# Optimization experiments

Measured on AMD Instinct MI355X. Metric: run time of the kernel, lower is better.

The kernel has to match this reference:

```python
import jax, jax.numpy as jnp
import numpy as np

B, C, H, W = 4, 512, 64, 64
D = C // 8  # inter_channels = 64


def setup_inputs() -> dict:
    key = jax.random.key(0)
    ks = jax.random.split(key, 10)
    s = 1.0 / np.sqrt(C)
    so = 1.0 / np.sqrt(D)
    return {
        "x": jax.random.normal(ks[0], (B, C, H, W), dtype=jnp.float32),
        "Wq": jax.random.normal(ks[1], (D, C), dtype=jnp.float32) * s,
        "bq": jnp.zeros((D,), dtype=jnp.float32),
        "Wk": jax.random.normal(ks[2], (D, C), dtype=jnp.float32) * s,
        "bk": jnp.zeros((D,), dtype=jnp.float32),
        "Wv": jax.random.normal(ks[3], (D, C), dtype=jnp.float32) * s,
        "bv": jnp.zeros((D,), dtype=jnp.float32),
        "Wo": jax.random.normal(ks[4], (C, D), dtype=jnp.float32) * so,
        "bo": jnp.zeros((C,), dtype=jnp.float32),
        "gamma": jnp.zeros((1,), dtype=jnp.float32),
    }


def reference(x, Wq, bq, Wk, bk, Wv, bv, Wo, bo, gamma):
    b, c, h, w = x.shape
    n = h * w
    xf = x.reshape(b, c, n)  # (B, C, N)
    # 1x1 convs == channel-mixing matmuls
    q = jnp.einsum("dc,bcn->bnd", Wq, xf) + bq              # (B, N, D)
    k = jnp.einsum("dc,bcn->bdn", Wk, xf) + bk[:, None]      # (B, D, N)
    v = jnp.einsum("dc,bcn->bnd", Wv, xf) + bv               # (B, N, D)
    scores = jnp.einsum("bnd,bdm->bnm", q, k)                # (B, N, N)
    weights = jax.nn.softmax(scores, axis=-1)
    attended = jnp.einsum("bnm,bmd->bnd", weights, v)        # (B, N, D)
    out = jnp.einsum("cd,bnd->bcn", Wo, attended) + bo[:, None]
    out = out.reshape(b, c, h, w)
    return gamma[0] * out + x
```

## Files before the change

### kernel.cpp

```cpp
#include <hip/hip_runtime.h>

#define NB 4
#define CH 512
#define NN 4096
#define DD 64

typedef __attribute__((ext_vector_type(8))) short bf16x8;
typedef __attribute__((ext_vector_type(4))) float f32x4;

#define MFMA(a, b, c) __builtin_amdgcn_mfma_f32_16x16x32_bf16((a), (b), (c), 0, 0, 0)

__device__ inline unsigned short f2bf(float f) {
    unsigned int u = __builtin_bit_cast(unsigned int, f);
    unsigned int r = u + 0x7fffu + ((u >> 16) & 1u);
    return (unsigned short)(r >> 16);
}

__device__ inline float bf2f(unsigned short u) {
    return __builtin_bit_cast(float, ((unsigned int)u) << 16);
}

__device__ inline bf16x8 ld8(const unsigned short* p) {
    return *reinterpret_cast<const bf16x8*>(p);
}

__global__ __launch_bounds__(256) void convert_w(
    const float* __restrict__ Wq, const float* __restrict__ Wk,
    const float* __restrict__ Wv, const float* __restrict__ Wo,
    unsigned short* __restrict__ oq, unsigned short* __restrict__ ok,
    unsigned short* __restrict__ ov, unsigned short* __restrict__ oo) {
    int i = blockIdx.x * 256 + threadIdx.x;
    oq[i] = f2bf(Wq[i]);
    ok[i] = f2bf(Wk[i]);
    ov[i] = f2bf(Wv[i]);
    oo[i] = f2bf(Wo[i]);
}

__global__ __launch_bounds__(256) void qkv_kernel(
    const float* __restrict__ x,
    const unsigned short* __restrict__ Wq, const unsigned short* __restrict__ Wk,
    const unsigned short* __restrict__ Wv,
    const float* __restrict__ bq, const float* __restrict__ bk, const float* __restrict__ bv,
    unsigned short* __restrict__ Q, unsigned short* __restrict__ K,
    unsigned short* __restrict__ VT) {
    const int b = blockIdx.x >> 8;
    const int n0 = (blockIdx.x & 255) * 16;
    const int t = threadIdx.x;
    const int lane = t & 63, w = t >> 6;
    const int l15 = lane & 15, g = lane >> 4;

    __shared__ char smraw[36864];
    unsigned short (*sxT)[520] = (unsigned short(*)[520])smraw;
    float* red = (float*)smraw;

    {
        const int cbase = t >> 2;
        const int nq = (t & 3) * 4;
#pragma unroll
        for (int p = 0; p < 8; ++p) {
            int c = p * 64 + cbase;
            float4 v = *reinterpret_cast<const float4*>(
                &x[((size_t)(b * CH + c)) * NN + n0 + nq]);
            sxT[nq + 0][c] = f2bf(v.x);
            sxT[nq + 1][c] = f2bf(v.y);
            sxT[nq + 2][c] = f2bf(v.z);
            sxT[nq + 3][c] = f2bf(v.w);
        }
    }
    __syncthreads();

    f32x4 accQ[4], accK[4], accV[4];
    const f32x4 z = {0.f, 0.f, 0.f, 0.f};
#pragma unroll
    for (int i = 0; i < 4; ++i) { accQ[i] = z; accK[i] = z; accV[i] = z; }

    const int wc = w * 128;
#pragma unroll
    for (int i = 0; i < 4; ++i) {
        int c = wc + i * 32 + 8 * g;
        bf16x8 ax = ld8(&sxT[l15][c]);
#pragma unroll
        for (int dt = 0; dt < 4; ++dt) {
            int d = dt * 16 + l15;
            accQ[dt] = MFMA(ax, ld8(&Wq[d * CH + c]), accQ[dt]);
            accK[dt] = MFMA(ax, ld8(&Wk[d * CH + c]), accK[dt]);
            accV[dt] = MFMA(ld8(&Wv[d * CH + c]), ax, accV[dt]);
        }
    }
    __syncthreads();

    if (w > 0) {
        float* dst = &red[((w - 1) * 64 + lane) * 48];
#pragma unroll
        for (int i = 0; i < 4; ++i) {
            *reinterpret_cast<f32x4*>(&dst[i * 4]) = accQ[i];
            *reinterpret_cast<f32x4*>(&dst[16 + i * 4]) = accK[i];
            *reinterpret_cast<f32x4*>(&dst[32 + i * 4]) = accV[i];
        }
    }
    __syncthreads();
    if (w == 0) {
#pragma unroll
        for (int ww = 0; ww < 3; ++ww) {
            const float* src = &red[(ww * 64 + lane) * 48];
#pragma unroll
            for (int i = 0; i < 4; ++i) {
                accQ[i] += *reinterpret_cast<const f32x4*>(&src[i * 4]);
                accK[i] += *reinterpret_cast<const f32x4*>(&src[16 + i * 4]);
                accV[i] += *reinterpret_cast<const f32x4*>(&src[32 + i * 4]);
            }
        }
#pragma unroll
        for (int dt = 0; dt < 4; ++dt) {
            int d = dt * 16 + l15;
            float biasq = bq[d], biask = bk[d];
#pragma unroll
            for (int r = 0; r < 4; ++r) {
                int n = n0 + 4 * g + r;
                Q[((size_t)b * NN + n) * DD + d] = f2bf(accQ[dt][r] + biasq);
                K[((size_t)b * NN + n) * DD + d] = f2bf(accK[dt][r] + biask);
            }
        }
#pragma unroll
        for (int dt = 0; dt < 4; ++dt) {
#pragma unroll
            for (int r = 0; r < 4; ++r) {
                int d = dt * 16 + 4 * g + r;
                VT[((size_t)b * DD + d) * NN + n0 + l15] = f2bf(accV[dt][r] + bv[d]);
            }
        }
    }
}

__global__ __launch_bounds__(256) void attn_kernel(
    const unsigned short* __restrict__ Q, const unsigned short* __restrict__ K,
    const unsigned short* __restrict__ VT,
    unsigned short* __restrict__ PO, float* __restrict__ PML, int KVLEN) {
    const int s = blockIdx.x >> 8;
    const int bq_ = blockIdx.x & 255;
    const int b = bq_ >> 6;
    const int n0 = (bq_ & 63) * 64;
    const int t = threadIdx.x;
    const int lane = t & 63, w = t >> 6;
    const int l15 = lane & 15, g = lane >> 4;

    __shared__ unsigned short sK[64][72];
    __shared__ unsigned short sVT[64][72];
    __shared__ unsigned short sP[4][16][76];

    const int qrow = n0 + 16 * w + l15;
    bf16x8 qf0 = ld8(&Q[((size_t)b * NN + qrow) * DD + 0 + 8 * g]);
    bf16x8 qf1 = ld8(&Q[((size_t)b * NN + qrow) * DD + 32 + 8 * g]);

    f32x4 oacc[4];
    const f32x4 z = {0.f, 0.f, 0.f, 0.f};
#pragma unroll
    for (int i = 0; i < 4; ++i) oacc[i] = z;
    float m_run[4], l_run[4];
#pragma unroll
    for (int r = 0; r < 4; ++r) { m_run[r] = -1e30f; l_run[r] = 0.f; }

    const int kv_begin = s * KVLEN;
    const int kv_end = kv_begin + KVLEN;
    for (int m0 = kv_begin; m0 < kv_end; m0 += 64) {
        {
            int row = t >> 2, c16 = (t & 3) * 16;
            const unsigned short* kp = &K[((size_t)b * NN + m0 + row) * DD + c16];
            *reinterpret_cast<bf16x8*>(&sK[row][c16]) = ld8(kp);
            *reinterpret_cast<bf16x8*>(&sK[row][c16 + 8]) = ld8(kp + 8);
            const unsigned short* vp = &VT[((size_t)b * DD + row) * NN + m0 + c16];
            *reinterpret_cast<bf16x8*>(&sVT[row][c16]) = ld8(vp);
            *reinterpret_cast<bf16x8*>(&sVT[row][c16 + 8]) = ld8(vp + 8);
        }
        __syncthreads();

        f32x4 sv[4];
#pragma unroll
        for (int ct = 0; ct < 4; ++ct) sv[ct] = z;
#pragma unroll
        for (int ct = 0; ct < 4; ++ct) {
            bf16x8 kf0 = ld8(&sK[ct * 16 + l15][0 + 8 * g]);
            sv[ct] = MFMA(qf0, kf0, sv[ct]);
            bf16x8 kf1 = ld8(&sK[ct * 16 + l15][32 + 8 * g]);
            sv[ct] = MFMA(qf1, kf1, sv[ct]);
        }

        float corr[4];
#pragma unroll
        for (int r = 0; r < 4; ++r) {
            float mx = fmaxf(fmaxf(sv[0][r], sv[1][r]), fmaxf(sv[2][r], sv[3][r]));
#pragma unroll
            for (int d_ = 8; d_ >= 1; d_ >>= 1) mx = fmaxf(mx, __shfl_xor(mx, d_, 64));
            float mnew = fmaxf(m_run[r], mx);
            float c_ = __expf(m_run[r] - mnew);
            float rs = 0.f;
#pragma unroll
            for (int ct = 0; ct < 4; ++ct) {
                float p = __expf(sv[ct][r] - mnew);
                sv[ct][r] = p;
                rs += p;
            }
#pragma unroll
            for (int d_ = 8; d_ >= 1; d_ >>= 1) rs += __shfl_xor(rs, d_, 64);
            l_run[r] = l_run[r] * c_ + rs;
            m_run[r] = mnew;
            corr[r] = c_;
        }
#pragma unroll
        for (int dt = 0; dt < 4; ++dt)
#pragma unroll
            for (int r = 0; r < 4; ++r) oacc[dt][r] *= corr[r];

#pragma unroll
        for (int ct = 0; ct < 4; ++ct)
#pragma unroll
            for (int r = 0; r < 4; ++r)
                sP[w][4 * g + r][ct * 16 + l15] = f2bf(sv[ct][r]);

#pragma unroll
        for (int kk = 0; kk < 2; ++kk) {
            bf16x8 pf = ld8(&sP[w][l15][kk * 32 + 8 * g]);
#pragma unroll
            for (int dt = 0; dt < 4; ++dt) {
                bf16x8 vf = ld8(&sVT[dt * 16 + l15][kk * 32 + 8 * g]);
                oacc[dt] = MFMA(pf, vf, oacc[dt]);
            }
        }
        __syncthreads();
    }

#pragma unroll
    for (int r = 0; r < 4; ++r) {
        int n = n0 + 16 * w + 4 * g + r;
        size_t rowidx = (size_t)s * NB * NN + (size_t)b * NN + n;
#pragma unroll
        for (int dt = 0; dt < 4; ++dt)
            PO[rowidx * DD + dt * 16 + l15] = f2bf(oacc[dt][r]);
        if (l15 == 0) {
            PML[rowidx * 2 + 0] = m_run[r];
            PML[rowidx * 2 + 1] = l_run[r];
        }
    }
}

__global__ __launch_bounds__(256) void out_fused(
    const unsigned short* __restrict__ Wo, const unsigned short* __restrict__ PO,
    const float* __restrict__ PML, const float* __restrict__ bo,
    const float* __restrict__ gamma, const float* __restrict__ x,
    float* __restrict__ out, int S) {
    const int bid = blockIdx.x;
    const int b = bid >> 8;
    const int rest = bid & 255;
    const int n0 = (rest >> 2) * 64;
    const int c0 = (rest & 3) * 128;
    const int t = threadIdx.x;
    const int lane = t & 63, w = t >> 6;
    const int l15 = lane & 15, g = lane >> 4;

    __shared__ unsigned short sATT[64][72];

    {
        const int row = t >> 2;
        const int dq = (t & 3) * 16;
        const size_t base = (size_t)b * NN + n0 + row;
        float m = -1e30f;
        for (int s = 0; s < S; ++s)
            m = fmaxf(m, PML[((size_t)s * NB * NN + base) * 2]);
        float acc[16];
#pragma unroll
        for (int j = 0; j < 16; ++j) acc[j] = 0.f;
        float l = 0.f;
        for (int s = 0; s < S; ++s) {
            size_t rowidx = (size_t)s * NB * NN + base;
            float ms = PML[rowidx * 2 + 0];
            float ls = PML[rowidx * 2 + 1];
            float wgt = __expf(ms - m);
            l += wgt * ls;
            bf16x8 a0 = ld8(&PO[rowidx * DD + dq]);
            bf16x8 a1 = ld8(&PO[rowidx * DD + dq + 8]);
#pragma unroll
            for (int j = 0; j < 8; ++j) {
                acc[j] += wgt * bf2f((unsigned short)a0[j]);
                acc[8 + j] += wgt * bf2f((unsigned short)a1[j]);
            }
        }
        float inv = 1.f / l;
        bf16x8 o0, o1;
#pragma unroll
        for (int j = 0; j < 8; ++j) {
            o0[j] = (short)f2bf(acc[j] * inv);
            o1[j] = (short)f2bf(acc[8 + j] * inv);
        }
        *reinterpret_cast<bf16x8*>(&sATT[row][dq]) = o0;
        *reinterpret_cast<bf16x8*>(&sATT[row][dq + 8]) = o1;
    }
    __syncthreads();

    const int cw = c0 + w * 32;
    f32x4 acc2[2][4];
    const f32x4 z = {0.f, 0.f, 0.f, 0.f};
#pragma unroll
    for (int i = 0; i < 2; ++i)
#pragma unroll
        for (int j = 0; j < 4; ++j) acc2[i][j] = z;

#pragma unroll
    for (int kk = 0; kk < 2; ++kk) {
        bf16x8 af[2], bfr[4];
#pragma unroll
        for (int ct = 0; ct < 2; ++ct)
            af[ct] = ld8(&Wo[(cw + ct * 16 + l15) * DD + kk * 32 + 8 * g]);
#pragma unroll
        for (int nt = 0; nt < 4; ++nt)
            bfr[nt] = ld8(&sATT[nt * 16 + l15][kk * 32 + 8 * g]);
#pragma unroll
        for (int ct = 0; ct < 2; ++ct)
#pragma unroll
            for (int nt = 0; nt < 4; ++nt) acc2[ct][nt] = MFMA(af[ct], bfr[nt], acc2[ct][nt]);
    }

    float gm = gamma[0];
#pragma unroll
    for (int ct = 0; ct < 2; ++ct) {
        int c = cw + ct * 16 + 4 * g;
#pragma unroll
        for (int r = 0; r < 4; ++r) {
            float bias = bo[c + r];
#pragma unroll
            for (int nt = 0; nt < 4; ++nt) {
                int n = n0 + nt * 16 + l15;
                size_t idx = ((size_t)b * CH + c + r) * NN + n;
                out[idx] = gm * (acc2[ct][nt][r] + bias) + x[idx];
            }
        }
    }
}

extern "C" void kernel_launch(void* const* d_in, const int* in_sizes, int n_in,
                              void* d_out, int out_size, void* d_ws, size_t ws_size,
                              hipStream_t stream) {
    const float* x = (const float*)d_in[0];
    const float* Wq = (const float*)d_in[1];
    const float* bq = (const float*)d_in[2];
    const float* Wk = (const float*)d_in[3];
    const float* bk = (const float*)d_in[4];
    const float* Wv = (const float*)d_in[5];
    const float* bv = (const float*)d_in[6];
    const float* Wo = (const float*)d_in[7];
    const float* bo = (const float*)d_in[8];
    const float* gamma = (const float*)d_in[9];
    float* out = (float*)d_out;

    char* ws = (char*)d_ws;
    unsigned short* Wq_bf = (unsigned short*)(ws + 0);
    unsigned short* Wk_bf = (unsigned short*)(ws + 65536);
    unsigned short* Wv_bf = (unsigned short*)(ws + 131072);
    unsigned short* Wo_bf = (unsigned short*)(ws + 196608);
    unsigned short* Qb = (unsigned short*)(ws + 262144);
    unsigned short* Kb = (unsigned short*)(ws + 262144 + 2097152);
    unsigned short* VTb = (unsigned short*)(ws + 262144 + 2 * 2097152);
    const size_t po_off = 262144 + 3ull * 2097152;

    int S = 8;
    while (S > 1 &&
           ws_size < po_off + (size_t)S * (2097152ull + 131072ull))
        S >>= 1;
    unsigned short* PO = (unsigned short*)(ws + po_off);
    float* PML = (float*)(ws + po_off + (size_t)S * 2097152ull);

    hipLaunchKernelGGL(convert_w, dim3(128), dim3(256), 0, stream,
                       Wq, Wk, Wv, Wo, Wq_bf, Wk_bf, Wv_bf, Wo_bf);
    hipLaunchKernelGGL(qkv_kernel, dim3(1024), dim3(256), 0, stream,
                       x, Wq_bf, Wk_bf, Wv_bf, bq, bk, bv, Qb, Kb, VTb);
    hipLaunchKernelGGL(attn_kernel, dim3(256 * S), dim3(256), 0, stream,
                       Qb, Kb, VTb, PO, PML, NN / S);
    hipLaunchKernelGGL(out_fused, dim3(1024), dim3(256), 0, stream,
                       Wo_bf, PO, PML, bo, gamma, x, out, S);
}
```

Baseline: 214.4 us.

## Prefetch KV tiles, lazy softmax rescale, parallel QKV reduction, fewer splits

The attention kernel now loads the next K/V tile into registers while the current tile is being computed. It rescales the running max lazily, only when some row's new max exceeds the stored one by more than 8, and it defers the row-sum shuffle reduction to the end of the kernel. P is converted to bf16 by truncation instead of round-to-nearest. In the QKV kernel the cross-wave reduction and output writes are split across all four waves instead of being done by wave 0 alone, and the KV split count drops from 8 to 4, giving fewer partial outputs to merge but fewer blocks per launch.

```diff
diff --git a/kernel.cpp b/kernel.cpp
--- a/kernel.cpp
+++ b/kernel.cpp
@@ -14,6 +14,10 @@
     unsigned int u = __builtin_bit_cast(unsigned int, f);
     unsigned int r = u + 0x7fffu + ((u >> 16) & 1u);
     return (unsigned short)(r >> 16);
+}
+
+__device__ inline unsigned short f2bf_trunc(float f) {
+    return (unsigned short)(__builtin_bit_cast(unsigned int, f) >> 16);
 }
 
 __device__ inline float bf2f(unsigned short u) {
@@ -49,9 +53,9 @@
     const int lane = t & 63, w = t >> 6;
     const int l15 = lane & 15, g = lane >> 4;
 
-    __shared__ char smraw[36864];
+    __shared__ char smraw[49152];
     unsigned short (*sxT)[520] = (unsigned short(*)[520])smraw;
-    float* red = (float*)smraw;
+    float (*red)[4][64][12] = (float(*)[4][64][12])smraw;
 
     {
         const int cbase = t >> 2;
@@ -89,45 +93,38 @@
     }
     __syncthreads();
 
-    if (w > 0) {
-        float* dst = &red[((w - 1) * 64 + lane) * 48];
-#pragma unroll
-        for (int i = 0; i < 4; ++i) {
-            *reinterpret_cast<f32x4*>(&dst[i * 4]) = accQ[i];
-            *reinterpret_cast<f32x4*>(&dst[16 + i * 4]) = accK[i];
-            *reinterpret_cast<f32x4*>(&dst[32 + i * 4]) = accV[i];
-        }
+#pragma unroll
+    for (int dt = 0; dt < 4; ++dt) {
+        float* dst = &red[dt][w][lane][0];
+        *reinterpret_cast<f32x4*>(dst + 0) = accQ[dt];
+        *reinterpret_cast<f32x4*>(dst + 4) = accK[dt];
+        *reinterpret_cast<f32x4*>(dst + 8) = accV[dt];
     }
     __syncthreads();
-    if (w == 0) {
-#pragma unroll
-        for (int ww = 0; ww < 3; ++ww) {
-            const float* src = &red[(ww * 64 + lane) * 48];
-#pragma unroll
-            for (int i = 0; i < 4; ++i) {
-                accQ[i] += *reinterpret_cast<const f32x4*>(&src[i * 4]);
-                accK[i] += *reinterpret_cast<const f32x4*>(&src[16 + i * 4]);
-                accV[i] += *reinterpret_cast<const f32x4*>(&src[32 + i * 4]);
-            }
-        }
-#pragma unroll
-        for (int dt = 0; dt < 4; ++dt) {
-            int d = dt * 16 + l15;
-            float biasq = bq[d], biask = bk[d];
-#pragma unroll
-            for (int r = 0; r < 4; ++r) {
-                int n = n0 + 4 * g + r;
-                Q[((size_t)b * NN + n) * DD + d] = f2bf(accQ[dt][r] + biasq);
-                K[((size_t)b * NN + n) * DD + d] = f2bf(accK[dt][r] + biask);
-            }
-        }
-#pragma unroll
-        for (int dt = 0; dt < 4; ++dt) {
-#pragma unroll
-            for (int r = 0; r < 4; ++r) {
-                int d = dt * 16 + 4 * g + r;
-                VT[((size_t)b * DD + d) * NN + n0 + l15] = f2bf(accV[dt][r] + bv[d]);
-            }
+
+    f32x4 q = *reinterpret_cast<const f32x4*>(&red[w][0][lane][0]);
+    f32x4 k = *reinterpret_cast<const f32x4*>(&red[w][0][lane][4]);
+    f32x4 v = *reinterpret_cast<const f32x4*>(&red[w][0][lane][8]);
+#pragma unroll
+    for (int src = 1; src < 4; ++src) {
+        const float* sp = &red[w][src][lane][0];
+        q += *reinterpret_cast<const f32x4*>(sp + 0);
+        k += *reinterpret_cast<const f32x4*>(sp + 4);
+        v += *reinterpret_cast<const f32x4*>(sp + 8);
+    }
+    {
+        int d = w * 16 + l15;
+        float biasq = bq[d], biask = bk[d];
+#pragma unroll
+        for (int r = 0; r < 4; ++r) {
+            int n = n0 + 4 * g + r;
+            Q[((size_t)b * NN + n) * DD + d] = f2bf(q[r] + biasq);
+            K[((size_t)b * NN + n) * DD + d] = f2bf(k[r] + biask);
+        }
+#pragma unroll
+        for (int r = 0; r < 4; ++r) {
+            int dv = w * 16 + 4 * g + r;
+            VT[((size_t)b * DD + dv) * NN + n0 + l15] = f2bf(v[r] + bv[dv]);
         }
     }
 }
@@ -156,23 +153,35 @@
     const f32x4 z = {0.f, 0.f, 0.f, 0.f};
 #pragma unroll
     for (int i = 0; i < 4; ++i) oacc[i] = z;
-    float m_run[4], l_run[4];
-#pragma unroll
-    for (int r = 0; r < 4; ++r) { m_run[r] = -1e30f; l_run[r] = 0.f; }
+    float m_run[4], l_part[4];
+#pragma unroll
+    for (int r = 0; r < 4; ++r) { m_run[r] = -1e30f; l_part[r] = 0.f; }
 
     const int kv_begin = s * KVLEN;
     const int kv_end = kv_begin + KVLEN;
+    const int srow = t >> 2, sc16 = (t & 3) * 16;
+
+    bf16x8 pk0, pk1, pv0, pv1;
+    {
+        const unsigned short* kp = &K[((size_t)b * NN + kv_begin + srow) * DD + sc16];
+        pk0 = ld8(kp); pk1 = ld8(kp + 8);
+        const unsigned short* vp = &VT[((size_t)b * DD + srow) * NN + kv_begin + sc16];
+        pv0 = ld8(vp); pv1 = ld8(vp + 8);
+    }
+
     for (int m0 = kv_begin; m0 < kv_end; m0 += 64) {
-        {
-            int row = t >> 2, c16 = (t & 3) * 16;
-            const unsigned short* kp = &K[((size_t)b * NN + m0 + row) * DD + c16];
-            *reinterpret_cast<bf16x8*>(&sK[row][c16]) = ld8(kp);
-            *reinterpret_cast<bf16x8*>(&sK[row][c16 + 8]) = ld8(kp + 8);
-            const unsigned short* vp = &VT[((size_t)b * DD + row) * NN + m0 + c16];
-            *reinterpret_cast<bf16x8*>(&sVT[row][c16]) = ld8(vp);
-            *reinterpret_cast<bf16x8*>(&sVT[row][c16 + 8]) = ld8(vp + 8);
-        }
+        *reinterpret_cast<bf16x8*>(&sK[srow][sc16]) = pk0;
+        *reinterpret_cast<bf16x8*>(&sK[srow][sc16 + 8]) = pk1;
+        *reinterpret_cast<bf16x8*>(&sVT[srow][sc16]) = pv0;
+        *reinterpret_cast<bf16x8*>(&sVT[srow][sc16 + 8]) = pv1;
         __syncthreads();
+
+        if (m0 + 64 < kv_end) {
+            const unsigned short* kp = &K[((size_t)b * NN + m0 + 64 + srow) * DD + sc16];
+            pk0 = ld8(kp); pk1 = ld8(kp + 8);
+            const unsigned short* vp = &VT[((size_t)b * DD + srow) * NN + m0 + 64 + sc16];
+            pv0 = ld8(vp); pv1 = ld8(vp + 8);
+        }
 
         f32x4 sv[4];
 #pragma unroll
@@ -185,37 +194,42 @@
             sv[ct] = MFMA(qf1, kf1, sv[ct]);
         }
 
-        float corr[4];
-#pragma unroll
-        for (int r = 0; r < 4; ++r) {
-            float mx = fmaxf(fmaxf(sv[0][r], sv[1][r]), fmaxf(sv[2][r], sv[3][r]));
-#pragma unroll
-            for (int d_ = 8; d_ >= 1; d_ >>= 1) mx = fmaxf(mx, __shfl_xor(mx, d_, 64));
-            float mnew = fmaxf(m_run[r], mx);
-            float c_ = __expf(m_run[r] - mnew);
-            float rs = 0.f;
-#pragma unroll
-            for (int ct = 0; ct < 4; ++ct) {
-                float p = __expf(sv[ct][r] - mnew);
-                sv[ct][r] = p;
-                rs += p;
+        float ownmax[4];
+        bool ok = true;
+#pragma unroll
+        for (int r = 0; r < 4; ++r) {
+            ownmax[r] = fmaxf(fmaxf(sv[0][r], sv[1][r]), fmaxf(sv[2][r], sv[3][r]));
+            ok = ok && (ownmax[r] <= m_run[r] + 8.f);
+        }
+        if (!__all(ok)) {
+#pragma unroll
+            for (int r = 0; r < 4; ++r) {
+                float mx = ownmax[r];
+#pragma unroll
+                for (int d_ = 8; d_ >= 1; d_ >>= 1) mx = fmaxf(mx, __shfl_xor(mx, d_, 64));
+                float mnew = fmaxf(m_run[r], mx);
+                float c_ = __expf(m_run[r] - mnew);
+                m_run[r] = mnew;
+                l_part[r] *= c_;
+#pragma unroll
+                for (int dt = 0; dt < 4; ++dt) oacc[dt][r] *= c_;
             }
-#pragma unroll
-            for (int d_ = 8; d_ >= 1; d_ >>= 1) rs += __shfl_xor(rs, d_, 64);
-            l_run[r] = l_run[r] * c_ + rs;
-            m_run[r] = mnew;
-            corr[r] = c_;
-        }
-#pragma unroll
-        for (int dt = 0; dt < 4; ++dt)
-#pragma unroll
-            for (int r = 0; r < 4; ++r) oacc[dt][r] *= corr[r];
+        }
+#pragma unroll
+        for (int r = 0; r < 4; ++r) {
+            float p0 = __expf(sv[0][r] - m_run[r]);
+            float p1 = __expf(sv[1][r] - m_run[r]);
+            float p2 = __expf(sv[2][r] - m_run[r]);
+            float p3 = __expf(sv[3][r] - m_run[r]);
+            sv[0][r] = p0; sv[1][r] = p1; sv[2][r] = p2; sv[3][r] = p3;
+            l_part[r] += (p0 + p1) + (p2 + p3);
+        }
 
 #pragma unroll
         for (int ct = 0; ct < 4; ++ct)
 #pragma unroll
             for (int r = 0; r < 4; ++r)
-                sP[w][4 * g + r][ct * 16 + l15] = f2bf(sv[ct][r]);
+                sP[w][4 * g + r][ct * 16 + l15] = f2bf_trunc(sv[ct][r]);
 
 #pragma unroll
         for (int kk = 0; kk < 2; ++kk) {
@@ -231,6 +245,9 @@
 
 #pragma unroll
     for (int r = 0; r < 4; ++r) {
+        float lt = l_part[r];
+#pragma unroll
+        for (int d_ = 8; d_ >= 1; d_ >>= 1) lt += __shfl_xor(lt, d_, 64);
         int n = n0 + 16 * w + 4 * g + r;
         size_t rowidx = (size_t)s * NB * NN + (size_t)b * NN + n;
 #pragma unroll
@@ -238,7 +255,7 @@
             PO[rowidx * DD + dt * 16 + l15] = f2bf(oacc[dt][r]);
         if (l15 == 0) {
             PML[rowidx * 2 + 0] = m_run[r];
-            PML[rowidx * 2 + 1] = l_run[r];
+            PML[rowidx * 2 + 1] = lt;
         }
     }
 }
@@ -361,7 +378,7 @@
     unsigned short* VTb = (unsigned short*)(ws + 262144 + 2 * 2097152);
     const size_t po_off = 262144 + 3ull * 2097152;
 
-    int S = 8;
+    int S = 4;
     while (S > 1 &&
            ws_size < po_off + (size_t)S * (2097152ull + 131072ull))
         S >>= 1;
```

Result: faster. 195.6 us (-8.8%).
